# Kernel tuning notes

Hardware: AMD Instinct MI355X
Metric: run time of the kernel (lower is better)

## Reference

```python
import jax, jax.numpy as jnp
import numpy as np

NUM_INPUT = 700
NUM_HIDDEN = 256
NUM_OUTPUT = 20
WIN = 50
BATCH = 512
DELAYS = (0, 16, 32)
MAX_D = 32
N_LAYERS = 2
THRESH = 0.3
ALPHA = 0.8  # membrane decay tau_m
LENS = 0.5   # surrogate-gradient window

@jax.custom_vjp
def spike_fn(u):
    # Heaviside with rectangular surrogate gradient (ActFun in the torch repo)
    return (u > 0.0).astype(u.dtype)

def _spike_fwd(u):
    return spike_fn(u), u

def _spike_bwd(u, g):
    return (g * (jnp.abs(u) < LENS).astype(u.dtype),)

spike_fn.defvjp(_spike_fwd, _spike_bwd)


def setup_inputs() -> dict:
    key = jax.random.key(0)
    ks = jax.random.split(key, 6)
    def init(k, shape, fan_in):
        return (jax.random.normal(k, shape, jnp.float32) / np.sqrt(fan_in)).astype(jnp.float32)
    return {
        "x":  jax.random.uniform(ks[0], (BATCH, WIN, NUM_INPUT), jnp.float32),
        # one input Linear per delay: [n_delays, H, In]
        "Wd": init(ks[1], (len(DELAYS), NUM_HIDDEN, NUM_INPUT), NUM_INPUT),
        "bd": jnp.zeros((len(DELAYS), NUM_HIDDEN), jnp.float32),
        # per-layer feedforward and recurrent weights
        "Wf": init(ks[2], (N_LAYERS, NUM_HIDDEN, NUM_HIDDEN), NUM_HIDDEN),
        "bf": jnp.zeros((N_LAYERS, NUM_HIDDEN), jnp.float32),
        "Wr": init(ks[3], (N_LAYERS, NUM_HIDDEN, NUM_HIDDEN), NUM_HIDDEN),
        # readout
        "Wo": init(ks[4], (NUM_OUTPUT, NUM_HIDDEN), NUM_HIDDEN),
        "bo": jnp.zeros((NUM_OUTPUT,), jnp.float32),
    }


def _forward(x, Wd, bd, Wf, bf, Wr, Wo, bo):
    B, win, _ = x.shape
    # extended_input: zeros for the first MAX_D steps, then the input
    ext = jnp.pad(x, ((0, 0), (MAX_D, 0), (0, 0)))
    # Precompute summed delayed input currents for all timesteps at once.
    cur = jnp.zeros((B, win, NUM_HIDDEN), x.dtype)
    for i, d in enumerate(DELAYS):
        sl = jax.lax.dynamic_slice_in_dim(ext, MAX_D - d, win, axis=1)
        cur = cur + jnp.einsum('bti,hi->bth', sl, Wd[i]) + bd[i]

    def step(carry, cur_t):
        mems, spks, o_mem, o_spk, o_sum, out_mot = carry
        prev = cur_t  # [B, H] summed delayed-input activations
        new_m, new_s = [], []
        for l in range(N_LAYERS):
            m = mems[l] * ALPHA * (1.0 - spks[l]) + prev @ Wf[l].T + bf[l] + spks[l] @ Wr[l].T
            s = spike_fn(m - THRESH)
            new_m.append(m)
            new_s.append(s)
            prev = s
        o_mem = o_mem * ALPHA * (1.0 - o_spk) + prev @ Wo.T + bo
        o_spk = spike_fn(o_mem - THRESH)
        o_sum = o_sum + o_spk
        out_mot = out_mot + jax.nn.softmax(o_mem, axis=1)
        return (jnp.stack(new_m), jnp.stack(new_s), o_mem, o_spk, o_sum, out_mot), None

    z = jnp.zeros((B, NUM_OUTPUT), x.dtype)
    zh = jnp.zeros((N_LAYERS, B, NUM_HIDDEN), x.dtype)
    carry0 = (zh, zh, z, z, z, z)
    carry, _ = jax.lax.scan(step, carry0, jnp.swapaxes(cur, 0, 1))
    _, _, _, _, o_sum, out_mot = carry
    return (o_sum / win, out_mot)


def reference(x, Wd, bd, Wf, bf, Wr, Wo, bo):
    return _forward(x, Wd, bd, Wf, bf, Wr, Wo, bo)
```

## Files before the change

### kernel.cpp

```cpp
#include <hip/hip_runtime.h>
#include <cstddef>

#define CUR_ELEMS (25600 * 256)
#define WROWS 65792

__global__ __launch_bounds__(256) void k0_transpose(
    const float* __restrict__ Wf, const float* __restrict__ Wr,
    const float* __restrict__ Wo, float* __restrict__ ws) {
  int tid = blockIdx.x * blockDim.x + threadIdx.x;
  float* Wr0T = ws + CUR_ELEMS;
  float* Wf1T = Wr0T + WROWS;
  float* Wr1T = Wf1T + WROWS;
  float* WoT  = Wr1T + WROWS;
  if (tid < WROWS) {
    int k = tid >> 8, h = tid & 255;
    Wr0T[tid] = (k < 256) ? Wr[h * 256 + k] : 0.f;
  } else if (tid < 2 * WROWS) {
    int i = tid - WROWS; int k = i >> 8, h = i & 255;
    Wf1T[i] = (k < 256) ? Wf[65536 + h * 256 + k] : 0.f;
  } else if (tid < 3 * WROWS) {
    int i = tid - 2 * WROWS; int k = i >> 8, h = i & 255;
    Wr1T[i] = (k < 256) ? Wr[65536 + h * 256 + k] : 0.f;
  } else if (tid < 3 * WROWS + 5140) {
    int i = tid - 3 * WROWS; int k = i / 20, j = i - k * 20;
    WoT[i] = (k < 256) ? Wo[j * 256 + k] : 0.f;
  }
}

__global__ __launch_bounds__(256) void k1_cur(
    const float* __restrict__ x, const float* __restrict__ Wd,
    const float* __restrict__ bd, float* __restrict__ cur) {
  __shared__ float As[2][16][132];
  __shared__ float Bs[2][16][132];
  const int t  = 49 - blockIdx.y;
  const int bt = blockIdx.x >> 1, ht = blockIdx.x & 1;
  const int b0 = bt * 128, h0 = ht * 128;
  const int tid = threadIdx.x;
  const int tx = tid & 15, ty = tid >> 4;
  const int r = tid & 127, half = tid >> 7;
  const int kk0a = half * 8;

  float acc[8][8];
#pragma unroll
  for (int i = 0; i < 8; ++i)
#pragma unroll
    for (int j = 0; j < 8; ++j) acc[i][j] = 0.f;

  const int DEL[3] = {0, 16, 32};
#pragma unroll 1
  for (int di = 0; di < 3; ++di) {
    const int d = DEL[di];
    if (t < d) continue;
    const int tsrc = t - d;
    const float* Arow = x + ((size_t)(b0 + r) * 50 + tsrc) * 700;
    const float* Brow = Wd + (size_t)di * 179200 + (size_t)(h0 + r) * 700;
    float4 pa0, pa1, pb0, pb1;
    pa0 = *(const float4*)(Arow + kk0a);
    pa1 = *(const float4*)(Arow + kk0a + 4);
    pb0 = *(const float4*)(Brow + kk0a);
    pb1 = *(const float4*)(Brow + kk0a + 4);
    As[0][kk0a + 0][r] = pa0.x; As[0][kk0a + 1][r] = pa0.y;
    As[0][kk0a + 2][r] = pa0.z; As[0][kk0a + 3][r] = pa0.w;
    As[0][kk0a + 4][r] = pa1.x; As[0][kk0a + 5][r] = pa1.y;
    As[0][kk0a + 6][r] = pa1.z; As[0][kk0a + 7][r] = pa1.w;
    Bs[0][kk0a + 0][r] = pb0.x; Bs[0][kk0a + 1][r] = pb0.y;
    Bs[0][kk0a + 2][r] = pb0.z; Bs[0][kk0a + 3][r] = pb0.w;
    Bs[0][kk0a + 4][r] = pb1.x; Bs[0][kk0a + 5][r] = pb1.y;
    Bs[0][kk0a + 6][r] = pb1.z; Bs[0][kk0a + 7][r] = pb1.w;
    pa0 = *(const float4*)(Arow + 16 + kk0a);
    pa1 = *(const float4*)(Arow + 16 + kk0a + 4);
    pb0 = *(const float4*)(Brow + 16 + kk0a);
    pb1 = *(const float4*)(Brow + 16 + kk0a + 4);
    __syncthreads();
#pragma unroll 1
    for (int c = 0; c < 44; ++c) {
      const int cb = c & 1, nb = cb ^ 1;
      if (c < 43) {
        As[nb][kk0a + 0][r] = pa0.x; As[nb][kk0a + 1][r] = pa0.y;
        As[nb][kk0a + 2][r] = pa0.z; As[nb][kk0a + 3][r] = pa0.w;
        As[nb][kk0a + 4][r] = pa1.x; As[nb][kk0a + 5][r] = pa1.y;
        As[nb][kk0a + 6][r] = pa1.z; As[nb][kk0a + 7][r] = pa1.w;
        Bs[nb][kk0a + 0][r] = pb0.x; Bs[nb][kk0a + 1][r] = pb0.y;
        Bs[nb][kk0a + 2][r] = pb0.z; Bs[nb][kk0a + 3][r] = pb0.w;
        Bs[nb][kk0a + 4][r] = pb1.x; Bs[nb][kk0a + 5][r] = pb1.y;
        Bs[nb][kk0a + 6][r] = pb1.z; Bs[nb][kk0a + 7][r] = pb1.w;
      }
      if (c < 42) {
        const int i0 = (c + 2) * 16 + kk0a, i1 = i0 + 4;
        pa0 = (i0 + 3 < 700) ? *(const float4*)(Arow + i0)
                             : make_float4(0.f, 0.f, 0.f, 0.f);
        pa1 = (i1 + 3 < 700) ? *(const float4*)(Arow + i1)
                             : make_float4(0.f, 0.f, 0.f, 0.f);
        pb0 = (i0 + 3 < 700) ? *(const float4*)(Brow + i0)
                             : make_float4(0.f, 0.f, 0.f, 0.f);
        pb1 = (i1 + 3 < 700) ? *(const float4*)(Brow + i1)
                             : make_float4(0.f, 0.f, 0.f, 0.f);
      }
#pragma unroll
      for (int kk = 0; kk < 16; ++kk) {
        const float4 a0 = *(const float4*)&As[cb][kk][ty * 4];
        const float4 a1 = *(const float4*)&As[cb][kk][64 + ty * 4];
        const float4 c0 = *(const float4*)&Bs[cb][kk][tx * 4];
        const float4 c1 = *(const float4*)&Bs[cb][kk][64 + tx * 4];
        const float ar[8] = {a0.x, a0.y, a0.z, a0.w, a1.x, a1.y, a1.z, a1.w};
        const float br[8] = {c0.x, c0.y, c0.z, c0.w, c1.x, c1.y, c1.z, c1.w};
#pragma unroll
        for (int rr = 0; rr < 8; ++rr)
#pragma unroll
          for (int cc = 0; cc < 8; ++cc) acc[rr][cc] += ar[rr] * br[cc];
      }
      __syncthreads();
    }
  }
  float bias[8];
#pragma unroll
  for (int q = 0; q < 2; ++q)
#pragma unroll
    for (int c = 0; c < 4; ++c) {
      const int col = h0 + q * 64 + tx * 4 + c;
      bias[q * 4 + c] = bd[col] + bd[256 + col] + bd[512 + col];
    }
#pragma unroll
  for (int p = 0; p < 2; ++p)
#pragma unroll
    for (int rr = 0; rr < 4; ++rr) {
      const int row = b0 + p * 64 + ty * 4 + rr;
      float* dst = cur + ((size_t)t * 512 + row) * 256 + h0;
      const int ai = p * 4 + rr;
      float4 v0 = make_float4(acc[ai][0] + bias[0], acc[ai][1] + bias[1],
                              acc[ai][2] + bias[2], acc[ai][3] + bias[3]);
      float4 v1 = make_float4(acc[ai][4] + bias[4], acc[ai][5] + bias[5],
                              acc[ai][6] + bias[6], acc[ai][7] + bias[7]);
      *(float4*)(dst + tx * 4) = v0;
      *(float4*)(dst + 64 + tx * 4) = v1;
    }
}

__global__ __launch_bounds__(256) void k1b_ff0(
    const float* __restrict__ Wf, const float* __restrict__ bf,
    float* __restrict__ cur) {
  __shared__ float As[16][68];
  __shared__ float Bs[16][260];
  const int m0 = blockIdx.x * 64;
  const int tid = threadIdx.x;
  const int tx = tid & 15, ty = tid >> 4;
  const int lr = tid & 63, akk = (tid >> 6) * 4;

  float acc[4][16];
#pragma unroll
  for (int i = 0; i < 4; ++i)
#pragma unroll
    for (int j = 0; j < 16; ++j) acc[i][j] = 0.f;

#pragma unroll 1
  for (int k0 = 0; k0 < 256; k0 += 16) {
    float4 av = *(const float4*)(cur + (size_t)(m0 + lr) * 256 + k0 + akk);
    As[akk + 0][lr] = av.x; As[akk + 1][lr] = av.y;
    As[akk + 2][lr] = av.z; As[akk + 3][lr] = av.w;
#pragma unroll
    for (int e = 0; e < 4; ++e) {
      const int hh = e * 64 + lr;
      float4 bv = *(const float4*)(Wf + (size_t)hh * 256 + k0 + akk);
      Bs[akk + 0][hh] = bv.x; Bs[akk + 1][hh] = bv.y;
      Bs[akk + 2][hh] = bv.z; Bs[akk + 3][hh] = bv.w;
    }
    __syncthreads();
#pragma unroll
    for (int kk = 0; kk < 16; ++kk) {
      const float4 a = *(const float4*)&As[kk][ty * 4];
      const float ar[4] = {a.x, a.y, a.z, a.w};
#pragma unroll
      for (int q = 0; q < 4; ++q) {
        const float4 bq = *(const float4*)&Bs[kk][q * 64 + tx * 4];
        const float br[4] = {bq.x, bq.y, bq.z, bq.w};
#pragma unroll
        for (int rr = 0; rr < 4; ++rr)
#pragma unroll
          for (int cc = 0; cc < 4; ++cc)
            acc[rr][q * 4 + cc] += ar[rr] * br[cc];
      }
    }
    __syncthreads();
  }
  float bias[16];
#pragma unroll
  for (int q = 0; q < 4; ++q)
#pragma unroll
    for (int c = 0; c < 4; ++c) bias[q * 4 + c] = bf[q * 64 + tx * 4 + c];
#pragma unroll
  for (int rr = 0; rr < 4; ++rr) {
    float* dst = cur + (size_t)(m0 + ty * 4 + rr) * 256;
#pragma unroll
    for (int q = 0; q < 4; ++q) {
      float4 v = make_float4(acc[rr][q * 4 + 0] + bias[q * 4 + 0],
                             acc[rr][q * 4 + 1] + bias[q * 4 + 1],
                             acc[rr][q * 4 + 2] + bias[q * 4 + 2],
                             acc[rr][q * 4 + 3] + bias[q * 4 + 3]);
      *(float4*)(dst + q * 64 + tx * 4) = v;
    }
  }
}

__device__ __forceinline__ void load8rows(const float* __restrict__ W,
                                          const int* LC, int j, int l4,
                                          float4* w) {
  const int4 a = *(const int4*)(LC + j);
  const int4 c = *(const int4*)(LC + j + 4);
  w[0] = *(const float4*)(W + a.x + l4);
  w[1] = *(const float4*)(W + a.y + l4);
  w[2] = *(const float4*)(W + a.z + l4);
  w[3] = *(const float4*)(W + a.w + l4);
  w[4] = *(const float4*)(W + c.x + l4);
  w[5] = *(const float4*)(W + c.y + l4);
  w[6] = *(const float4*)(W + c.z + l4);
  w[7] = *(const float4*)(W + c.w + l4);
}

__device__ __forceinline__ void add8rows(float4& acc, const float4* w) {
  float4 t0, t1, t2, t3;
  t0.x = w[0].x + w[1].x; t0.y = w[0].y + w[1].y; t0.z = w[0].z + w[1].z; t0.w = w[0].w + w[1].w;
  t1.x = w[2].x + w[3].x; t1.y = w[2].y + w[3].y; t1.z = w[2].z + w[3].z; t1.w = w[2].w + w[3].w;
  t2.x = w[4].x + w[5].x; t2.y = w[4].y + w[5].y; t2.z = w[4].z + w[5].z; t2.w = w[4].w + w[5].w;
  t3.x = w[6].x + w[7].x; t3.y = w[6].y + w[7].y; t3.z = w[6].z + w[7].z; t3.w = w[6].w + w[7].w;
  t0.x += t1.x; t0.y += t1.y; t0.z += t1.z; t0.w += t1.w;
  t2.x += t3.x; t2.y += t3.y; t2.z += t3.z; t2.w += t3.w;
  acc.x += t0.x + t2.x; acc.y += t0.y + t2.y;
  acc.z += t0.z + t2.z; acc.w += t0.w + t2.w;
}

__device__ __forceinline__ float4 gather_rows(const float* __restrict__ W,
                                              const int* LC, int n, int l4) {
  float4 acc = make_float4(0.f, 0.f, 0.f, 0.f);
  const int G = n >> 3;
  if (G == 0) return acc;
  float4 w0[8], w1[8], w2[8], w3[8];
  load8rows(W, LC, 0,  l4, w0);
  load8rows(W, LC, 8,  l4, w1);
  load8rows(W, LC, 16, l4, w2);
  load8rows(W, LC, 24, l4, w3);
  int g = 4;
  for (; g + 4 <= G; g += 4) {
    add8rows(acc, w0); load8rows(W, LC, (g + 0) * 8, l4, w0);
    add8rows(acc, w1); load8rows(W, LC, (g + 1) * 8, l4, w1);
    add8rows(acc, w2); load8rows(W, LC, (g + 2) * 8, l4, w2);
    add8rows(acc, w3); load8rows(W, LC, (g + 3) * 8, l4, w3);
  }
  add8rows(acc, w0); add8rows(acc, w1);
  add8rows(acc, w2); add8rows(acc, w3);
  return acc;
}

__device__ __forceinline__ float add8o(const float* w) {
  return ((w[0] + w[1]) + (w[2] + w[3])) + ((w[4] + w[5]) + (w[6] + w[7]));
}

__global__ __launch_bounds__(64, 1) void k2_scan(
    const float* __restrict__ ff0, const float* __restrict__ Wr0T,
    const float* __restrict__ Wf1T, const float* __restrict__ Wr1T,
    const float* __restrict__ WoT, const float* __restrict__ bf,
    const float* __restrict__ bo, float* __restrict__ out) {
  __shared__ __align__(16) int LC0[288];
  __shared__ __align__(16) int LC1[288];
  __shared__ __align__(16) int LCb[280];
  __shared__ float WoTl[5140];
  __shared__ float obuf[20];
  const int b = blockIdx.x;
  const int lane = threadIdx.x;
  const int l4 = lane * 4;
  const unsigned long long lb = (1ull << lane) - 1ull;

  for (int i = lane; i < 1285; i += 64)
    *(float4*)(WoTl + 4 * i) = *(const float4*)(WoT + 4 * i);

  float4 m0 = make_float4(0.f, 0.f, 0.f, 0.f), m1 = m0;
  float4 s0v = m0, s1v = m0;
  const float4 bf1v = *(const float4*)(bf + 256 + l4);
  float omem = 0.f, ospk = 0.f, osum = 0.f, omot = 0.f;
  const float bov = (lane < 20) ? bo[lane] : 0.f;
  const int ro = lane / 3, rc = lane - ro * 3;
  int n0 = 0, n1g = 0, n1r = 0;

  const float* ffp = ff0 + (size_t)b * 256 + l4;
  float4 ff = *(const float4*)ffp;

#pragma unroll 1
  for (int t = 0; t < 50; ++t) {
    float4 ffn = ff;
    if (t < 49) ffn = *(const float4*)(ffp + (size_t)(t + 1) * 131072);
    {
      const float4 g = gather_rows(Wr0T, LC0, n0, l4);
      m0.x = m0.x * 0.8f * (1.f - s0v.x) + ff.x + g.x;
      m0.y = m0.y * 0.8f * (1.f - s0v.y) + ff.y + g.y;
      m0.z = m0.z * 0.8f * (1.f - s0v.z) + ff.z + g.z;
      m0.w = m0.w * 0.8f * (1.f - s0v.w) + ff.w + g.w;
      s0v.x = (m0.x - 0.3f > 0.f) ? 1.f : 0.f;
      s0v.y = (m0.y - 0.3f > 0.f) ? 1.f : 0.f;
      s0v.z = (m0.z - 0.3f > 0.f) ? 1.f : 0.f;
      s0v.w = (m0.w - 0.3f > 0.f) ? 1.f : 0.f;
    }
    {
      const float sv[4] = {s0v.x, s0v.y, s0v.z, s0v.w};
      int base = 0;
#pragma unroll
      for (int q = 0; q < 4; ++q) {
        const bool sp = sv[q] > 0.f;
        const unsigned long long mk = __ballot(sp);
        const int pos = base + (int)__popcll(mk & lb);
        if (sp) LC0[pos] = (l4 + q) << 8;
        base += (int)__popcll(mk);
      }
      const int pad = (-base) & 31;
      if (lane < pad) LC0[base + lane] = 256 << 8;
      n0 = base + pad;
    }
    {
      const float4 g1 = gather_rows(Wf1T, LC0, n0, l4);
      const float4 g2 = gather_rows(Wr1T, LC1, n1g, l4);
      m1.x = m1.x * 0.8f * (1.f - s1v.x) + bf1v.x + g1.x + g2.x;
      m1.y = m1.y * 0.8f * (1.f - s1v.y) + bf1v.y + g1.y + g2.y;
      m1.z = m1.z * 0.8f * (1.f - s1v.z) + bf1v.z + g1.z + g2.z;
      m1.w = m1.w * 0.8f * (1.f - s1v.w) + bf1v.w + g1.w + g2.w;
      s1v.x = (m1.x - 0.3f > 0.f) ? 1.f : 0.f;
      s1v.y = (m1.y - 0.3f > 0.f) ? 1.f : 0.f;
      s1v.z = (m1.z - 0.3f > 0.f) ? 1.f : 0.f;
      s1v.w = (m1.w - 0.3f > 0.f) ? 1.f : 0.f;
    }
    {
      const float sv[4] = {s1v.x, s1v.y, s1v.z, s1v.w};
      int base = 0;
#pragma unroll
      for (int q = 0; q < 4; ++q) {
        const bool sp = sv[q] > 0.f;
        const unsigned long long mk = __ballot(sp);
        const int pos = base + (int)__popcll(mk & lb);
        if (sp) { LC1[pos] = (l4 + q) << 8; LCb[pos] = (l4 + q) * 20; }
        base += (int)__popcll(mk);
      }
      const int padg = (-base) & 31;
      if (lane < padg) LC1[base + lane] = 256 << 8;
      n1g = base + padg;
      const int rem = base % 24;
      const int padr = rem ? (24 - rem) : 0;
      if (lane < padr) LCb[base + lane] = 256 * 20;
      n1r = base + padr;
    }
    {
      float v = 0.f;
      if (lane < 60) {
        const int GR = n1r / 24;
        int j = rc;
        for (int g = 0; g < GR; ++g) {
          int idx[8]; float w[8];
#pragma unroll
          for (int u = 0; u < 8; ++u) idx[u] = LCb[j + 3 * u];
#pragma unroll
          for (int u = 0; u < 8; ++u) w[u] = WoTl[idx[u] + ro];
          v += add8o(w);
          j += 24;
        }
      }
      const float v1 = __shfl_down(v, 1);
      const float v2 = __shfl_down(v, 2);
      v += v1 + v2;
      if (rc == 0 && lane < 60) obuf[ro] = v;
      if (lane < 20) {
        const float oacc = bov + obuf[lane];
        omem = omem * 0.8f * (1.f - ospk) + oacc;
        ospk = (omem - 0.3f > 0.f) ? 1.f : 0.f;
        osum += ospk;
        obuf[lane] = omem;
      }
      if (lane < 20) {
        float ov[20];
#pragma unroll
        for (int j2 = 0; j2 < 20; ++j2) ov[j2] = obuf[j2];
        float mx = ov[0];
#pragma unroll
        for (int j2 = 1; j2 < 20; ++j2) mx = fmaxf(mx, ov[j2]);
        float sm = 0.f;
#pragma unroll
        for (int j2 = 0; j2 < 20; ++j2) sm += expf(ov[j2] - mx);
        omot += expf(omem - mx) / sm;
      }
    }
    ff = ffn;
  }
  if (lane < 20) {
    out[b * 20 + lane] = osum / 50.0f;
    out[10240 + b * 20 + lane] = omot;
  }
}

extern "C" void kernel_launch(void* const* d_in, const int* in_sizes, int n_in,
                              void* d_out, int out_size, void* d_ws, size_t ws_size,
                              hipStream_t stream) {
  const float* x  = (const float*)d_in[0];
  const float* Wd = (const float*)d_in[1];
  const float* bd = (const float*)d_in[2];
  const float* Wf = (const float*)d_in[3];
  const float* bf = (const float*)d_in[4];
  const float* Wr = (const float*)d_in[5];
  const float* Wo = (const float*)d_in[6];
  const float* bo = (const float*)d_in[7];
  float* out = (float*)d_out;
  float* ws  = (float*)d_ws;

  float* cur  = ws;
  float* Wr0T = ws + CUR_ELEMS;
  float* Wf1T = Wr0T + WROWS;
  float* Wr1T = Wf1T + WROWS;
  float* WoT  = Wr1T + WROWS;

  hipLaunchKernelGGL(k0_transpose, dim3(792), dim3(256), 0, stream, Wf, Wr, Wo, ws);
  hipLaunchKernelGGL(k1_cur, dim3(8, 50), dim3(256), 0, stream, x, Wd, bd, cur);
  hipLaunchKernelGGL(k1b_ff0, dim3(400), dim3(256), 0, stream, Wf, bf, cur);
  hipLaunchKernelGGL(k2_scan, dim3(512), dim3(64), 0, stream, cur, Wr0T, Wf1T,
                     Wr1T, WoT, bf, bo, out);
}
```

Measured before the change: 895.9 us.

## Load-balance delayed-input GEMM across blocks and interleave recurrent gathers

The input-current GEMM kernel used to launch one block per (timestep, tile), so blocks did one, two or three delay passes and the work was uneven. It now launches 248 blocks, each given one or two timesteps whose combined pass count is three or four. In the scan kernel, the recurrent gathers for layer 0 and layer 1 (Wr0T and Wr1T) are issued together through a new dual-gather helper so their memory loads overlap. This raises register pressure in the single-wave scan kernel, and some GEMM blocks still do more passes than others.

```diff
diff --git a/kernel.cpp b/kernel.cpp
--- a/kernel.cpp
+++ b/kernel.cpp
@@ -32,86 +32,21 @@
     const float* __restrict__ bd, float* __restrict__ cur) {
   __shared__ float As[2][16][132];
   __shared__ float Bs[2][16][132];
-  const int t  = 49 - blockIdx.y;
-  const int bt = blockIdx.x >> 1, ht = blockIdx.x & 1;
+  const int tile = blockIdx.x & 7;
+  const int u = blockIdx.x >> 3;
+  const int bt = tile >> 1, ht = tile & 1;
   const int b0 = bt * 128, h0 = ht * 128;
   const int tid = threadIdx.x;
   const int tx = tid & 15, ty = tid >> 4;
   const int r = tid & 127, half = tid >> 7;
   const int kk0a = half * 8;
 
-  float acc[8][8];
-#pragma unroll
-  for (int i = 0; i < 8; ++i)
-#pragma unroll
-    for (int j = 0; j < 8; ++j) acc[i][j] = 0.f;
-
-  const int DEL[3] = {0, 16, 32};
-#pragma unroll 1
-  for (int di = 0; di < 3; ++di) {
-    const int d = DEL[di];
-    if (t < d) continue;
-    const int tsrc = t - d;
-    const float* Arow = x + ((size_t)(b0 + r) * 50 + tsrc) * 700;
-    const float* Brow = Wd + (size_t)di * 179200 + (size_t)(h0 + r) * 700;
-    float4 pa0, pa1, pb0, pb1;
-    pa0 = *(const float4*)(Arow + kk0a);
-    pa1 = *(const float4*)(Arow + kk0a + 4);
-    pb0 = *(const float4*)(Brow + kk0a);
-    pb1 = *(const float4*)(Brow + kk0a + 4);
-    As[0][kk0a + 0][r] = pa0.x; As[0][kk0a + 1][r] = pa0.y;
-    As[0][kk0a + 2][r] = pa0.z; As[0][kk0a + 3][r] = pa0.w;
-    As[0][kk0a + 4][r] = pa1.x; As[0][kk0a + 5][r] = pa1.y;
-    As[0][kk0a + 6][r] = pa1.z; As[0][kk0a + 7][r] = pa1.w;
-    Bs[0][kk0a + 0][r] = pb0.x; Bs[0][kk0a + 1][r] = pb0.y;
-    Bs[0][kk0a + 2][r] = pb0.z; Bs[0][kk0a + 3][r] = pb0.w;
-    Bs[0][kk0a + 4][r] = pb1.x; Bs[0][kk0a + 5][r] = pb1.y;
-    Bs[0][kk0a + 6][r] = pb1.z; Bs[0][kk0a + 7][r] = pb1.w;
-    pa0 = *(const float4*)(Arow + 16 + kk0a);
-    pa1 = *(const float4*)(Arow + 16 + kk0a + 4);
-    pb0 = *(const float4*)(Brow + 16 + kk0a);
-    pb1 = *(const float4*)(Brow + 16 + kk0a + 4);
-    __syncthreads();
-#pragma unroll 1
-    for (int c = 0; c < 44; ++c) {
-      const int cb = c & 1, nb = cb ^ 1;
-      if (c < 43) {
-        As[nb][kk0a + 0][r] = pa0.x; As[nb][kk0a + 1][r] = pa0.y;
-        As[nb][kk0a + 2][r] = pa0.z; As[nb][kk0a + 3][r] = pa0.w;
-        As[nb][kk0a + 4][r] = pa1.x; As[nb][kk0a + 5][r] = pa1.y;
-        As[nb][kk0a + 6][r] = pa1.z; As[nb][kk0a + 7][r] = pa1.w;
-        Bs[nb][kk0a + 0][r] = pb0.x; Bs[nb][kk0a + 1][r] = pb0.y;
-        Bs[nb][kk0a + 2][r] = pb0.z; Bs[nb][kk0a + 3][r] = pb0.w;
-        Bs[nb][kk0a + 4][r] = pb1.x; Bs[nb][kk0a + 5][r] = pb1.y;
-        Bs[nb][kk0a + 6][r] = pb1.z; Bs[nb][kk0a + 7][r] = pb1.w;
-      }
-      if (c < 42) {
-        const int i0 = (c + 2) * 16 + kk0a, i1 = i0 + 4;
-        pa0 = (i0 + 3 < 700) ? *(const float4*)(Arow + i0)
-                             : make_float4(0.f, 0.f, 0.f, 0.f);
-        pa1 = (i1 + 3 < 700) ? *(const float4*)(Arow + i1)
-                             : make_float4(0.f, 0.f, 0.f, 0.f);
-        pb0 = (i0 + 3 < 700) ? *(const float4*)(Brow + i0)
-                             : make_float4(0.f, 0.f, 0.f, 0.f);
-        pb1 = (i1 + 3 < 700) ? *(const float4*)(Brow + i1)
-                             : make_float4(0.f, 0.f, 0.f, 0.f);
-      }
-#pragma unroll
-      for (int kk = 0; kk < 16; ++kk) {
-        const float4 a0 = *(const float4*)&As[cb][kk][ty * 4];
-        const float4 a1 = *(const float4*)&As[cb][kk][64 + ty * 4];
-        const float4 c0 = *(const float4*)&Bs[cb][kk][tx * 4];
-        const float4 c1 = *(const float4*)&Bs[cb][kk][64 + tx * 4];
-        const float ar[8] = {a0.x, a0.y, a0.z, a0.w, a1.x, a1.y, a1.z, a1.w};
-        const float br[8] = {c0.x, c0.y, c0.z, c0.w, c1.x, c1.y, c1.z, c1.w};
-#pragma unroll
-        for (int rr = 0; rr < 8; ++rr)
-#pragma unroll
-          for (int cc = 0; cc < 8; ++cc) acc[rr][cc] += ar[rr] * br[cc];
-      }
-      __syncthreads();
-    }
-  }
+  int tJ[2], nJ[2];
+  if (u < 6)       { tJ[0] = 32 + u;          nJ[0] = 3; tJ[1] = u;              nJ[1] = 1; }
+  else if (u < 9)  { tJ[0] = 26 + 2 * (u - 6); nJ[0] = 2; tJ[1] = 27 + 2 * (u - 6); nJ[1] = 2; }
+  else if (u < 21) { tJ[0] = 38 + (u - 9);    nJ[0] = 3; tJ[1] = 0;              nJ[1] = 0; }
+  else             { tJ[0] = 16 + (u - 21);   nJ[0] = 2; tJ[1] = 6 + (u - 21);   nJ[1] = 1; }
+
   float bias[8];
 #pragma unroll
   for (int q = 0; q < 2; ++q)
@@ -120,20 +55,99 @@
       const int col = h0 + q * 64 + tx * 4 + c;
       bias[q * 4 + c] = bd[col] + bd[256 + col] + bd[512 + col];
     }
-#pragma unroll
-  for (int p = 0; p < 2; ++p)
-#pragma unroll
-    for (int rr = 0; rr < 4; ++rr) {
-      const int row = b0 + p * 64 + ty * 4 + rr;
-      float* dst = cur + ((size_t)t * 512 + row) * 256 + h0;
-      const int ai = p * 4 + rr;
-      float4 v0 = make_float4(acc[ai][0] + bias[0], acc[ai][1] + bias[1],
-                              acc[ai][2] + bias[2], acc[ai][3] + bias[3]);
-      float4 v1 = make_float4(acc[ai][4] + bias[4], acc[ai][5] + bias[5],
-                              acc[ai][6] + bias[6], acc[ai][7] + bias[7]);
-      *(float4*)(dst + tx * 4) = v0;
-      *(float4*)(dst + 64 + tx * 4) = v1;
-    }
+
+  const int DEL[3] = {0, 16, 32};
+#pragma unroll 1
+  for (int jb = 0; jb < 2; ++jb) {
+    const int npass = nJ[jb];
+    if (npass == 0) continue;
+    const int t = tJ[jb];
+
+    float acc[8][8];
+#pragma unroll
+    for (int i = 0; i < 8; ++i)
+#pragma unroll
+      for (int j = 0; j < 8; ++j) acc[i][j] = 0.f;
+
+#pragma unroll 1
+    for (int di = 0; di < npass; ++di) {
+      const int tsrc = t - DEL[di];
+      const float* Arow = x + ((size_t)(b0 + r) * 50 + tsrc) * 700;
+      const float* Brow = Wd + (size_t)di * 179200 + (size_t)(h0 + r) * 700;
+      float4 pa0, pa1, pb0, pb1;
+      pa0 = *(const float4*)(Arow + kk0a);
+      pa1 = *(const float4*)(Arow + kk0a + 4);
+      pb0 = *(const float4*)(Brow + kk0a);
+      pb1 = *(const float4*)(Brow + kk0a + 4);
+      As[0][kk0a + 0][r] = pa0.x; As[0][kk0a + 1][r] = pa0.y;
+      As[0][kk0a + 2][r] = pa0.z; As[0][kk0a + 3][r] = pa0.w;
+      As[0][kk0a + 4][r] = pa1.x; As[0][kk0a + 5][r] = pa1.y;
+      As[0][kk0a + 6][r] = pa1.z; As[0][kk0a + 7][r] = pa1.w;
+      Bs[0][kk0a + 0][r] = pb0.x; Bs[0][kk0a + 1][r] = pb0.y;
+      Bs[0][kk0a + 2][r] = pb0.z; Bs[0][kk0a + 3][r] = pb0.w;
+      Bs[0][kk0a + 4][r] = pb1.x; Bs[0][kk0a + 5][r] = pb1.y;
+      Bs[0][kk0a + 6][r] = pb1.z; Bs[0][kk0a + 7][r] = pb1.w;
+      pa0 = *(const float4*)(Arow + 16 + kk0a);
+      pa1 = *(const float4*)(Arow + 16 + kk0a + 4);
+      pb0 = *(const float4*)(Brow + 16 + kk0a);
+      pb1 = *(const float4*)(Brow + 16 + kk0a + 4);
+      __syncthreads();
+#pragma unroll 1
+      for (int c = 0; c < 44; ++c) {
+        const int cb = c & 1, nb = cb ^ 1;
+        if (c < 43) {
+          As[nb][kk0a + 0][r] = pa0.x; As[nb][kk0a + 1][r] = pa0.y;
+          As[nb][kk0a + 2][r] = pa0.z; As[nb][kk0a + 3][r] = pa0.w;
+          As[nb][kk0a + 4][r] = pa1.x; As[nb][kk0a + 5][r] = pa1.y;
+          As[nb][kk0a + 6][r] = pa1.z; As[nb][kk0a + 7][r] = pa1.w;
+          Bs[nb][kk0a + 0][r] = pb0.x; Bs[nb][kk0a + 1][r] = pb0.y;
+          Bs[nb][kk0a + 2][r] = pb0.z; Bs[nb][kk0a + 3][r] = pb0.w;
+          Bs[nb][kk0a + 4][r] = pb1.x; Bs[nb][kk0a + 5][r] = pb1.y;
+          Bs[nb][kk0a + 6][r] = pb1.z; Bs[nb][kk0a + 7][r] = pb1.w;
+        }
+        if (c < 42) {
+          const int i0 = (c + 2) * 16 + kk0a, i1 = i0 + 4;
+          pa0 = (i0 + 3 < 700) ? *(const float4*)(Arow + i0)
+                               : make_float4(0.f, 0.f, 0.f, 0.f);
+          pa1 = (i1 + 3 < 700) ? *(const float4*)(Arow + i1)
+                               : make_float4(0.f, 0.f, 0.f, 0.f);
+          pb0 = (i0 + 3 < 700) ? *(const float4*)(Brow + i0)
+                               : make_float4(0.f, 0.f, 0.f, 0.f);
+          pb1 = (i1 + 3 < 700) ? *(const float4*)(Brow + i1)
+                               : make_float4(0.f, 0.f, 0.f, 0.f);
+        }
+#pragma unroll
+        for (int kk = 0; kk < 16; ++kk) {
+          const float4 a0 = *(const float4*)&As[cb][kk][ty * 4];
+          const float4 a1 = *(const float4*)&As[cb][kk][64 + ty * 4];
+          const float4 c0 = *(const float4*)&Bs[cb][kk][tx * 4];
+          const float4 c1 = *(const float4*)&Bs[cb][kk][64 + tx * 4];
+          const float ar[8] = {a0.x, a0.y, a0.z, a0.w, a1.x, a1.y, a1.z, a1.w};
+          const float br[8] = {c0.x, c0.y, c0.z, c0.w, c1.x, c1.y, c1.z, c1.w};
+#pragma unroll
+          for (int rr = 0; rr < 8; ++rr)
+#pragma unroll
+            for (int cc = 0; cc < 8; ++cc) acc[rr][cc] += ar[rr] * br[cc];
+        }
+        __syncthreads();
+      }
+    }
+#pragma unroll
+    for (int p = 0; p < 2; ++p)
+#pragma unroll
+      for (int rr = 0; rr < 4; ++rr) {
+        const int row = b0 + p * 64 + ty * 4 + rr;
+        float* dst = cur + ((size_t)t * 512 + row) * 256 + h0;
+        const int ai = p * 4 + rr;
+        float4 v0 = make_float4(acc[ai][0] + bias[0], acc[ai][1] + bias[1],
+                                acc[ai][2] + bias[2], acc[ai][3] + bias[3]);
+        float4 v1 = make_float4(acc[ai][4] + bias[4], acc[ai][5] + bias[5],
+                                acc[ai][6] + bias[6], acc[ai][7] + bias[7]);
+        *(float4*)(dst + tx * 4) = v0;
+        *(float4*)(dst + 64 + tx * 4) = v1;
+      }
+    __syncthreads();
+  }
 }
 
 __global__ __launch_bounds__(256) void k1b_ff0(
@@ -250,6 +264,40 @@
   return acc;
 }
 
+__device__ __forceinline__ void gather_dual(
+    const float* __restrict__ WA, const int* LA, int nA,
+    const float* __restrict__ WB, const int* LB, int nB, int l4,
+    float4& accA, float4& accB) {
+  const int GA = nA >> 3, GB = nB >> 3;
+  float4 wa0[8], wa1[8], wb0[8], wb1[8];
+  if (GA) { load8rows(WA, LA, 0, l4, wa0); load8rows(WA, LA, 8, l4, wa1); }
+  if (GB) { load8rows(WB, LB, 0, l4, wb0); load8rows(WB, LB, 8, l4, wb1); }
+  int ga = 0, gb = 0;
+  while (ga + 4 <= GA && gb + 4 <= GB) {
+    add8rows(accA, wa0); load8rows(WA, LA, (ga + 2) * 8, l4, wa0);
+    add8rows(accB, wb0); load8rows(WB, LB, (gb + 2) * 8, l4, wb0);
+    add8rows(accA, wa1); load8rows(WA, LA, (ga + 3) * 8, l4, wa1);
+    add8rows(accB, wb1); load8rows(WB, LB, (gb + 3) * 8, l4, wb1);
+    ga += 2; gb += 2;
+  }
+  if (GA) {
+    while (ga + 4 <= GA) {
+      add8rows(accA, wa0); load8rows(WA, LA, (ga + 2) * 8, l4, wa0);
+      add8rows(accA, wa1); load8rows(WA, LA, (ga + 3) * 8, l4, wa1);
+      ga += 2;
+    }
+    add8rows(accA, wa0); add8rows(accA, wa1);
+  }
+  if (GB) {
+    while (gb + 4 <= GB) {
+      add8rows(accB, wb0); load8rows(WB, LB, (gb + 2) * 8, l4, wb0);
+      add8rows(accB, wb1); load8rows(WB, LB, (gb + 3) * 8, l4, wb1);
+      gb += 2;
+    }
+    add8rows(accB, wb0); add8rows(accB, wb1);
+  }
+}
+
 __device__ __forceinline__ float add8o(const float* w) {
   return ((w[0] + w[1]) + (w[2] + w[3])) + ((w[4] + w[5]) + (w[6] + w[7]));
 }
@@ -287,12 +335,14 @@
   for (int t = 0; t < 50; ++t) {
     float4 ffn = ff;
     if (t < 49) ffn = *(const float4*)(ffp + (size_t)(t + 1) * 131072);
+    float4 g0 = make_float4(0.f, 0.f, 0.f, 0.f);
+    float4 gB = make_float4(0.f, 0.f, 0.f, 0.f);
+    gather_dual(Wr0T, LC0, n0, Wr1T, LC1, n1g, l4, g0, gB);
     {
-      const float4 g = gather_rows(Wr0T, LC0, n0, l4);
-      m0.x = m0.x * 0.8f * (1.f - s0v.x) + ff.x + g.x;
-      m0.y = m0.y * 0.8f * (1.f - s0v.y) + ff.y + g.y;
-      m0.z = m0.z * 0.8f * (1.f - s0v.z) + ff.z + g.z;
-      m0.w = m0.w * 0.8f * (1.f - s0v.w) + ff.w + g.w;
+      m0.x = m0.x * 0.8f * (1.f - s0v.x) + ff.x + g0.x;
+      m0.y = m0.y * 0.8f * (1.f - s0v.y) + ff.y + g0.y;
+      m0.z = m0.z * 0.8f * (1.f - s0v.z) + ff.z + g0.z;
+      m0.w = m0.w * 0.8f * (1.f - s0v.w) + ff.w + g0.w;
       s0v.x = (m0.x - 0.3f > 0.f) ? 1.f : 0.f;
       s0v.y = (m0.y - 0.3f > 0.f) ? 1.f : 0.f;
       s0v.z = (m0.z - 0.3f > 0.f) ? 1.f : 0.f;
@@ -315,11 +365,10 @@
     }
     {
       const float4 g1 = gather_rows(Wf1T, LC0, n0, l4);
-      const float4 g2 = gather_rows(Wr1T, LC1, n1g, l4);
-      m1.x = m1.x * 0.8f * (1.f - s1v.x) + bf1v.x + g1.x + g2.x;
-      m1.y = m1.y * 0.8f * (1.f - s1v.y) + bf1v.y + g1.y + g2.y;
-      m1.z = m1.z * 0.8f * (1.f - s1v.z) + bf1v.z + g1.z + g2.z;
-      m1.w = m1.w * 0.8f * (1.f - s1v.w) + bf1v.w + g1.w + g2.w;
+      m1.x = m1.x * 0.8f * (1.f - s1v.x) + bf1v.x + g1.x + gB.x;
+      m1.y = m1.y * 0.8f * (1.f - s1v.y) + bf1v.y + g1.y + gB.y;
+      m1.z = m1.z * 0.8f * (1.f - s1v.z) + bf1v.z + g1.z + gB.z;
+      m1.w = m1.w * 0.8f * (1.f - s1v.w) + bf1v.w + g1.w + gB.w;
       s1v.x = (m1.x - 0.3f > 0.f) ? 1.f : 0.f;
       s1v.y = (m1.y - 0.3f > 0.f) ? 1.f : 0.f;
       s1v.z = (m1.z - 0.3f > 0.f) ? 1.f : 0.f;
@@ -352,9 +401,9 @@
         for (int g = 0; g < GR; ++g) {
           int idx[8]; float w[8];
 #pragma unroll
-          for (int u = 0; u < 8; ++u) idx[u] = LCb[j + 3 * u];
-#pragma unroll
-          for (int u = 0; u < 8; ++u) w[u] = WoTl[idx[u] + ro];
+          for (int u2 = 0; u2 < 8; ++u2) idx[u2] = LCb[j + 3 * u2];
+#pragma unroll
+          for (int u2 = 0; u2 < 8; ++u2) w[u2] = WoTl[idx[u2] + ro];
           v += add8o(w);
           j += 24;
         }
@@ -412,7 +461,7 @@
   float* WoT  = Wr1T + WROWS;
 
   hipLaunchKernelGGL(k0_transpose, dim3(792), dim3(256), 0, stream, Wf, Wr, Wo, ws);
-  hipLaunchKernelGGL(k1_cur, dim3(8, 50), dim3(256), 0, stream, x, Wd, bd, cur);
+  hipLaunchKernelGGL(k1_cur, dim3(248), dim3(256), 0, stream, x, Wd, bd, cur);
   hipLaunchKernelGGL(k1b_ff0, dim3(400), dim3(256), 0, stream, Wf, bf, cur);
   hipLaunchKernelGGL(k2_scan, dim3(512), dim3(64), 0, stream, cur, Wr0T, Wf1T,
                      Wr1T, WoT, bf, bo, out);
```

Result: faster. 850.0 us (-5.1%).
